# Performance work log

Measured on AMD Instinct MI355X. Metric: run time of the kernel, lower is better.

The kernel has to match this reference:

```python
import jax, jax.numpy as jnp
import numpy as np

B, L, D = 32, 2048, 768
H = 512
EPS = 1e-5  # batch_norm eps (PyG MLP default norm)


def setup_inputs() -> dict:
    key = jax.random.key(0)
    ks = jax.random.split(key, 8)
    hidden = jax.random.normal(ks[0], (B, L, D), dtype=jnp.float32)
    attention_mask = jax.random.randint(ks[1], (B, L), 0, 2, dtype=jnp.int32)
    W1 = jax.random.normal(ks[2], (D, H), dtype=jnp.float32) * 0.02
    b1 = jnp.zeros((H,), dtype=jnp.float32)
    gamma = jnp.ones((H,), dtype=jnp.float32)
    beta = jnp.zeros((H,), dtype=jnp.float32)
    W2 = jax.random.normal(ks[3], (H, H), dtype=jnp.float32) * 0.02
    b2 = jnp.zeros((H,), dtype=jnp.float32)
    return {"hidden": hidden, "attention_mask": attention_mask,
            "W1": W1, "b1": b1, "gamma": gamma, "beta": beta,
            "W2": W2, "b2": b2}


def reference(hidden, attention_mask, W1, b1, gamma, beta, W2, b2):
    # Valid-token mask; pads are excluded from the batched graph's node set.
    m = attention_mask.astype(hidden.dtype)[..., None]  # (B, L, 1)
    n_valid = jnp.maximum(jnp.sum(m), 1.0)

    # MLP layer 1: Linear -> BatchNorm (stats over all valid nodes across the
    # whole batched graph, mirroring PyG MLP training-mode batch_norm) -> ReLU
    h = jnp.einsum('bld,dh->blh', hidden, W1) + b1  # (B, L, H)
    mean = jnp.sum(h * m, axis=(0, 1)) / n_valid
    var = jnp.sum(jnp.square(h - mean) * m, axis=(0, 1)) / n_valid
    h = (h - mean) * jax.lax.rsqrt(var + EPS) * gamma + beta
    h = jax.nn.relu(h)

    # MLP layer 2 (plain_last: no norm/act)
    out = jnp.einsum('blh,hk->blk', h, W2) + b2  # (B, L, H)

    # scores == ones -> segment softmax over each sequence's valid tokens is
    # uniform 1/n_b; scatter_add over batch ids == masked mean pool.
    counts = jnp.maximum(jnp.sum(m, axis=1), 1.0)  # (B, 1)
    pooled = jnp.sum(out * m, axis=1) / counts  # (B, H)
    return pooled
```

## Files before the change

### kernel.cpp

```cpp
#include <hip/hip_runtime.h>
#include <hip/hip_bf16.h>

#define Bn 32
#define Ln 2048
#define Dn 768
#define Hn 512
#define Mn (Bn*Ln)
#define EPSC 1e-5f

#define OFF_S1   0
#define OFF_S2   512
#define OFF_SC   1024
#define OFF_SH   1536
#define OFF_CNT  2048
#define OFF_PH   2304
#define ZERO_N   (OFF_PH + Bn*Hn)
#define OFF_W1T_BYTES  131072
#define OFF_H_BYTES    1048576

#define BM 128
#define BN2 256
#define BK 64
#define LDK 72

typedef __attribute__((ext_vector_type(8))) short bf16x8;
typedef __attribute__((ext_vector_type(4))) float f32x4;

static __device__ __forceinline__ unsigned short f2bf(float x) {
  __hip_bfloat16 h = __float2bfloat16(x);
  return *reinterpret_cast<unsigned short*>(&h);
}
static __device__ __forceinline__ float bf2f(unsigned short u) {
  return __uint_as_float(((unsigned int)u) << 16);
}

__global__ void zero_kernel(float* __restrict__ p, int n) {
  int i = blockIdx.x * 256 + threadIdx.x;
  if (i < n) p[i] = 0.f;
}

__global__ void count_kernel(const int* __restrict__ mask, float* __restrict__ cnt) {
  __shared__ int red[256];
  int b = blockIdx.x, t = threadIdx.x;
  int s = 0;
#pragma unroll
  for (int i = 0; i < 8; i++) s += mask[b * Ln + i * 256 + t];
  red[t] = s;
  __syncthreads();
  for (int off = 128; off > 0; off >>= 1) {
    if (t < off) red[t] += red[t + off];
    __syncthreads();
  }
  if (t == 0) cnt[b] = (float)red[0];
}

__global__ __launch_bounds__(256) void transpose_w1(
    const float* __restrict__ W1, unsigned short* __restrict__ W1t) {
  __shared__ float tile[32][33];
  int kx = blockIdx.x * 32;
  int nx = blockIdx.y * 32;
  int tx = threadIdx.x & 31, ty = threadIdx.x >> 5;
#pragma unroll
  for (int i = 0; i < 32; i += 8)
    tile[ty + i][tx] = W1[(size_t)(kx + ty + i) * Hn + nx + tx];
  __syncthreads();
#pragma unroll
  for (int i = 0; i < 32; i += 8)
    W1t[(size_t)(nx + ty + i) * Dn + kx + tx] = f2bf(tile[tx][ty + i]);
}

__global__ __launch_bounds__(512, 4) void gemm1_mfma(
    const float* __restrict__ A, const unsigned short* __restrict__ W1t,
    const float* __restrict__ b1, const int* __restrict__ mask,
    unsigned short* __restrict__ Hout,
    float* __restrict__ gsum, float* __restrict__ gsq)
{
  __shared__ unsigned short As[BM * LDK];
  __shared__ unsigned short Bs[BN2 * LDK];
  __shared__ float csum[BN2];
  __shared__ float csq[BN2];

  const int t = threadIdx.x;
  const int bx = blockIdx.x;
  const int by = blockIdx.y;
  const int bm0 = by * BM;
  const int bn0 = bx * BN2;

  const int w = t >> 6;
  const int lane = t & 63;
  const int wm0 = (w >> 2) * 64;
  const int wn0 = (w & 3) * 64;
  const int l15 = lane & 15;
  const int quad = lane >> 4;

  const int am = t >> 2;
  const int ak = (t & 3) * 16;
  const int bn = t >> 1;
  const int bk = (t & 1) * 32;

  const float* Ap = A + (size_t)(bm0 + am) * Dn + ak;
  const unsigned short* Bp = W1t + (size_t)(bn0 + bn) * Dn + bk;

  f32x4 acc[4][4];
#pragma unroll
  for (int i = 0; i < 4; i++)
#pragma unroll
    for (int j = 0; j < 4; j++) acc[i][j] = (f32x4){0.f, 0.f, 0.f, 0.f};

  for (int k0 = 0; k0 < Dn; k0 += BK) {
    float4 a0 = *(const float4*)(Ap + k0);
    float4 a1 = *(const float4*)(Ap + k0 + 4);
    float4 a2 = *(const float4*)(Ap + k0 + 8);
    float4 a3 = *(const float4*)(Ap + k0 + 12);
    uint4 bv0 = *(const uint4*)(Bp + k0);
    uint4 bv1 = *(const uint4*)(Bp + k0 + 8);
    uint4 bv2 = *(const uint4*)(Bp + k0 + 16);
    uint4 bv3 = *(const uint4*)(Bp + k0 + 24);
    __syncthreads();
    uint4 p0, p1;
    p0.x = (unsigned int)f2bf(a0.x) | ((unsigned int)f2bf(a0.y) << 16);
    p0.y = (unsigned int)f2bf(a0.z) | ((unsigned int)f2bf(a0.w) << 16);
    p0.z = (unsigned int)f2bf(a1.x) | ((unsigned int)f2bf(a1.y) << 16);
    p0.w = (unsigned int)f2bf(a1.z) | ((unsigned int)f2bf(a1.w) << 16);
    p1.x = (unsigned int)f2bf(a2.x) | ((unsigned int)f2bf(a2.y) << 16);
    p1.y = (unsigned int)f2bf(a2.z) | ((unsigned int)f2bf(a2.w) << 16);
    p1.z = (unsigned int)f2bf(a3.x) | ((unsigned int)f2bf(a3.y) << 16);
    p1.w = (unsigned int)f2bf(a3.z) | ((unsigned int)f2bf(a3.w) << 16);
    *(uint4*)&As[am * LDK + ak] = p0;
    *(uint4*)&As[am * LDK + ak + 8] = p1;
    *(uint4*)&Bs[bn * LDK + bk] = bv0;
    *(uint4*)&Bs[bn * LDK + bk + 8] = bv1;
    *(uint4*)&Bs[bn * LDK + bk + 16] = bv2;
    *(uint4*)&Bs[bn * LDK + bk + 24] = bv3;
    __syncthreads();
#pragma unroll
    for (int s = 0; s < 2; s++) {
      bf16x8 af[4], bf[4];
#pragma unroll
      for (int mt = 0; mt < 4; mt++)
        af[mt] = *(const bf16x8*)&As[(wm0 + mt * 16 + l15) * LDK + s * 32 + quad * 8];
#pragma unroll
      for (int nt = 0; nt < 4; nt++)
        bf[nt] = *(const bf16x8*)&Bs[(wn0 + nt * 16 + l15) * LDK + s * 32 + quad * 8];
#pragma unroll
      for (int mt = 0; mt < 4; mt++)
#pragma unroll
        for (int nt = 0; nt < 4; nt++)
          acc[mt][nt] = __builtin_amdgcn_mfma_f32_16x16x32_bf16(
              af[mt], bf[nt], acc[mt][nt], 0, 0, 0);
    }
  }

  if (t < BN2) { csum[t] = 0.f; csq[t] = 0.f; }
  __syncthreads();

  float mk[4][4];
#pragma unroll
  for (int mt = 0; mt < 4; mt++) {
    int4 mv = *(const int4*)(mask + bm0 + wm0 + mt * 16 + quad * 4);
    mk[mt][0] = (float)mv.x; mk[mt][1] = (float)mv.y;
    mk[mt][2] = (float)mv.z; mk[mt][3] = (float)mv.w;
  }

  const size_t cbase = ((size_t)(by * 2 + bx)) * 32768 + (size_t)w * 4096;
#pragma unroll
  for (int nt = 0; nt < 4; nt++) {
    const int nl = wn0 + nt * 16 + l15;
    const float bias = b1[bn0 + nl];
    float ps = 0.f, pq = 0.f;
#pragma unroll
    for (int mt = 0; mt < 4; mt++) {
      ushort4 st;
      float v0 = acc[mt][nt][0] + bias;
      float v1 = acc[mt][nt][1] + bias;
      float v2 = acc[mt][nt][2] + bias;
      float v3 = acc[mt][nt][3] + bias;
      ps += v0 * mk[mt][0] + v1 * mk[mt][1] + v2 * mk[mt][2] + v3 * mk[mt][3];
      pq += v0 * v0 * mk[mt][0] + v1 * v1 * mk[mt][1] +
            v2 * v2 * mk[mt][2] + v3 * v3 * mk[mt][3];
      st.x = f2bf(v0); st.y = f2bf(v1); st.z = f2bf(v2); st.w = f2bf(v3);
      *(ushort4*)&Hout[cbase + (size_t)(mt * 4 + nt) * 256 + lane * 4] = st;
    }
    atomicAdd(&csum[nl], ps);
    atomicAdd(&csq[nl], pq);
  }

  __syncthreads();
  if (t < BN2) {
    atomicAdd(&gsum[bn0 + t], csum[t]);
    atomicAdd(&gsq[bn0 + t], csq[t]);
  }
}

__global__ void finalize_kernel(float* __restrict__ ws,
                                const float* __restrict__ gamma,
                                const float* __restrict__ beta) {
  __shared__ float nv;
  int t = threadIdx.x;
  if (t == 0) {
    float s = 0.f;
    for (int i = 0; i < Bn; i++) s += ws[OFF_CNT + i];
    nv = fmaxf(s, 1.f);
  }
  __syncthreads();
  float inv = 1.f / nv;
  float m = ws[OFF_S1 + t] * inv;
  float var = ws[OFF_S2 + t] * inv - m * m;
  float istd = rsqrtf(fmaxf(var, 0.f) + EPSC);
  float sc = istd * gamma[t];
  ws[OFF_SC + t] = sc;
  ws[OFF_SH + t] = beta[t] - m * sc;
}

__global__ __launch_bounds__(256) void bnpool_kernel(
    const unsigned short* __restrict__ Hbuf, const int* __restrict__ mask,
    const float* __restrict__ sc, const float* __restrict__ sh,
    float* __restrict__ pooled)
{
  __shared__ float pool_c[BN2];
  __shared__ float mkf[BM];
  __shared__ float scs[BN2], shs[BN2];
  const int t = threadIdx.x;
  const int chunk = blockIdx.x;
  const int by = chunk >> 1, bx = chunk & 1;
  const int b = by >> 4;
  pool_c[t] = 0.f;
  if (t < BM) mkf[t] = (float)mask[by * BM + t];
  scs[t] = sc[bx * BN2 + t];
  shs[t] = sh[bx * BN2 + t];
  __syncthreads();
  const unsigned short* base = Hbuf + (size_t)chunk * 32768;
#pragma unroll 4
  for (int i = 0; i < 32; i++) {
    int o = (i * 256 + t) * 4;
    ushort4 hv = *(const ushort4*)(base + o);
    int lane = (o >> 2) & 63;
    int mtnt = (o >> 8) & 15;
    int w = o >> 12;
    int nl = (w & 3) * 64 + (mtnt & 3) * 16 + (lane & 15);
    int ml = (w >> 2) * 64 + (mtnt >> 2) * 16 + (lane >> 4) * 4;
    float4 mv = *(const float4*)&mkf[ml];
    float scv = scs[nl], shv = shs[nl];
    float s = 0.f;
    s = fmaf(fmaxf(fmaf(bf2f(hv.x), scv, shv), 0.f), mv.x, s);
    s = fmaf(fmaxf(fmaf(bf2f(hv.y), scv, shv), 0.f), mv.y, s);
    s = fmaf(fmaxf(fmaf(bf2f(hv.z), scv, shv), 0.f), mv.z, s);
    s = fmaf(fmaxf(fmaf(bf2f(hv.w), scv, shv), 0.f), mv.w, s);
    atomicAdd(&pool_c[nl], s);
  }
  __syncthreads();
  atomicAdd(&pooled[b * Hn + bx * BN2 + t], pool_c[t]);
}

__global__ __launch_bounds__(128) void final_kernel(
    const float* __restrict__ pooledh, const float* __restrict__ cnt,
    const float* __restrict__ W2, const float* __restrict__ b2,
    float* __restrict__ out)
{
  __shared__ float pr[Hn];
  int b = blockIdx.x >> 2;
  int cc = blockIdx.x & 3;
  int t = threadIdx.x;
  float nb = cnt[b];
  float inv = 1.f / fmaxf(nb, 1.f);
#pragma unroll
  for (int i = 0; i < 4; i++)
    pr[t + i * 128] = pooledh[b * Hn + t + i * 128] * inv;
  __syncthreads();
  int c = cc * 128 + t;
  float a = 0.f;
  for (int i = 0; i < Hn; i++)
    a = fmaf(pr[i], W2[(size_t)i * Hn + c], a);
  out[b * Hn + c] = a + b2[c] * (nb * inv);
}

extern "C" void kernel_launch(void* const* d_in, const int* in_sizes, int n_in,
                              void* d_out, int out_size, void* d_ws, size_t ws_size,
                              hipStream_t stream) {
  const float* hidden = (const float*)d_in[0];
  const int*   mask   = (const int*)d_in[1];
  const float* W1     = (const float*)d_in[2];
  const float* b1     = (const float*)d_in[3];
  const float* gamma  = (const float*)d_in[4];
  const float* beta   = (const float*)d_in[5];
  const float* W2     = (const float*)d_in[6];
  const float* b2     = (const float*)d_in[7];
  float* out = (float*)d_out;
  float* ws  = (float*)d_ws;
  unsigned short* W1t  = (unsigned short*)((char*)d_ws + OFF_W1T_BYTES);
  unsigned short* Hbuf = (unsigned short*)((char*)d_ws + OFF_H_BYTES);

  zero_kernel<<<(ZERO_N + 255) / 256, 256, 0, stream>>>(ws, ZERO_N);
  count_kernel<<<Bn, 256, 0, stream>>>(mask, ws + OFF_CNT);
  transpose_w1<<<dim3(Dn / 32, Hn / 32), 256, 0, stream>>>(W1, W1t);
  gemm1_mfma<<<dim3(Hn / BN2, Mn / BM), 512, 0, stream>>>(
      hidden, W1t, b1, mask, Hbuf, ws + OFF_S1, ws + OFF_S2);
  finalize_kernel<<<1, Hn, 0, stream>>>(ws, gamma, beta);
  bnpool_kernel<<<(Mn / BM) * (Hn / BN2), 256, 0, stream>>>(
      Hbuf, mask, ws + OFF_SC, ws + OFF_SH, ws + OFF_PH);
  final_kernel<<<Bn * 4, 128, 0, stream>>>(ws + OFF_PH, ws + OFF_CNT, W2, b2, out);
}
```

Measured before the change: 421.7 us.

## Shrink GEMM tile to 128x128, fuse launch prologue and BN finalize into pool

The first GEMM tile drops from 128x256 with 512 threads to 128x128 with 256 threads, and the occupancy hint changes. The zero and count kernels merge into one pre-kernel, and the BN finalize moves into the pool kernel so two launches disappear. The pool kernel now reduces per thread in registers and then across warps in shared memory, replacing per-element shared atomics. The final matvec uses four independent accumulators. Smaller tiles re-read the A matrix twice as often, and every pool block recomputes the scale and shift.

```diff
diff --git a/kernel.cpp b/kernel.cpp
--- a/kernel.cpp
+++ b/kernel.cpp
@@ -10,16 +10,13 @@
 
 #define OFF_S1   0
 #define OFF_S2   512
-#define OFF_SC   1024
-#define OFF_SH   1536
 #define OFF_CNT  2048
 #define OFF_PH   2304
-#define ZERO_N   (OFF_PH + Bn*Hn)
 #define OFF_W1T_BYTES  131072
 #define OFF_H_BYTES    1048576
 
 #define BM 128
-#define BN2 256
+#define BN2 128
 #define BK 64
 #define LDK 72
 
@@ -30,28 +27,34 @@
   __hip_bfloat16 h = __float2bfloat16(x);
   return *reinterpret_cast<unsigned short*>(&h);
 }
+static __device__ __forceinline__ unsigned int pk2(float lo, float hi) {
+  return (unsigned int)f2bf(lo) | ((unsigned int)f2bf(hi) << 16);
+}
 static __device__ __forceinline__ float bf2f(unsigned short u) {
   return __uint_as_float(((unsigned int)u) << 16);
 }
 
-__global__ void zero_kernel(float* __restrict__ p, int n) {
-  int i = blockIdx.x * 256 + threadIdx.x;
-  if (i < n) p[i] = 0.f;
-}
-
-__global__ void count_kernel(const int* __restrict__ mask, float* __restrict__ cnt) {
-  __shared__ int red[256];
-  int b = blockIdx.x, t = threadIdx.x;
-  int s = 0;
-#pragma unroll
-  for (int i = 0; i < 8; i++) s += mask[b * Ln + i * 256 + t];
-  red[t] = s;
-  __syncthreads();
-  for (int off = 128; off > 0; off >>= 1) {
-    if (t < off) red[t] += red[t + off];
+__global__ __launch_bounds__(256) void pre_kernel(const int* __restrict__ mask,
+                                                  float* __restrict__ ws) {
+  int blk = blockIdx.x, t = threadIdx.x;
+  if (blk < Bn) {
+    __shared__ int red[256];
+    int s = 0;
+#pragma unroll
+    for (int i = 0; i < 8; i++) s += mask[blk * Ln + i * 256 + t];
+    red[t] = s;
     __syncthreads();
-  }
-  if (t == 0) cnt[b] = (float)red[0];
+    for (int off = 128; off > 0; off >>= 1) {
+      if (t < off) red[t] += red[t + off];
+      __syncthreads();
+    }
+    if (t == 0) ws[OFF_CNT + blk] = (float)red[0];
+  } else {
+#pragma unroll
+    for (int i = 0; i < 4; i++) ws[OFF_S1 + i * 256 + t] = 0.f;
+#pragma unroll
+    for (int i = 0; i < 64; i++) ws[OFF_PH + i * 256 + t] = 0.f;
+  }
 }
 
 __global__ __launch_bounds__(256) void transpose_w1(
@@ -69,7 +72,7 @@
     W1t[(size_t)(nx + ty + i) * Dn + kx + tx] = f2bf(tile[tx][ty + i]);
 }
 
-__global__ __launch_bounds__(512, 4) void gemm1_mfma(
+__global__ __launch_bounds__(256, 3) void gemm1_mfma(
     const float* __restrict__ A, const unsigned short* __restrict__ W1t,
     const float* __restrict__ b1, const int* __restrict__ mask,
     unsigned short* __restrict__ Hout,
@@ -88,18 +91,16 @@
 
   const int w = t >> 6;
   const int lane = t & 63;
-  const int wm0 = (w >> 2) * 64;
-  const int wn0 = (w & 3) * 64;
+  const int wm0 = (w >> 1) * 64;
+  const int wn0 = (w & 1) * 64;
   const int l15 = lane & 15;
   const int quad = lane >> 4;
 
-  const int am = t >> 2;
-  const int ak = (t & 3) * 16;
-  const int bn = t >> 1;
-  const int bk = (t & 1) * 32;
+  const int am = t >> 1;
+  const int ak = (t & 1) * 32;
 
   const float* Ap = A + (size_t)(bm0 + am) * Dn + ak;
-  const unsigned short* Bp = W1t + (size_t)(bn0 + bn) * Dn + bk;
+  const unsigned short* Bp = W1t + (size_t)(bn0 + am) * Dn + ak;
 
   f32x4 acc[4][4];
 #pragma unroll
@@ -108,30 +109,23 @@
     for (int j = 0; j < 4; j++) acc[i][j] = (f32x4){0.f, 0.f, 0.f, 0.f};
 
   for (int k0 = 0; k0 < Dn; k0 += BK) {
-    float4 a0 = *(const float4*)(Ap + k0);
-    float4 a1 = *(const float4*)(Ap + k0 + 4);
-    float4 a2 = *(const float4*)(Ap + k0 + 8);
-    float4 a3 = *(const float4*)(Ap + k0 + 12);
-    uint4 bv0 = *(const uint4*)(Bp + k0);
-    uint4 bv1 = *(const uint4*)(Bp + k0 + 8);
-    uint4 bv2 = *(const uint4*)(Bp + k0 + 16);
-    uint4 bv3 = *(const uint4*)(Bp + k0 + 24);
+    float4 av[8];
+#pragma unroll
+    for (int i = 0; i < 8; i++) av[i] = *(const float4*)(Ap + k0 + i * 4);
+    uint4 bv[4];
+#pragma unroll
+    for (int j = 0; j < 4; j++) bv[j] = *(const uint4*)(Bp + k0 + j * 8);
     __syncthreads();
-    uint4 p0, p1;
-    p0.x = (unsigned int)f2bf(a0.x) | ((unsigned int)f2bf(a0.y) << 16);
-    p0.y = (unsigned int)f2bf(a0.z) | ((unsigned int)f2bf(a0.w) << 16);
-    p0.z = (unsigned int)f2bf(a1.x) | ((unsigned int)f2bf(a1.y) << 16);
-    p0.w = (unsigned int)f2bf(a1.z) | ((unsigned int)f2bf(a1.w) << 16);
-    p1.x = (unsigned int)f2bf(a2.x) | ((unsigned int)f2bf(a2.y) << 16);
-    p1.y = (unsigned int)f2bf(a2.z) | ((unsigned int)f2bf(a2.w) << 16);
-    p1.z = (unsigned int)f2bf(a3.x) | ((unsigned int)f2bf(a3.y) << 16);
-    p1.w = (unsigned int)f2bf(a3.z) | ((unsigned int)f2bf(a3.w) << 16);
-    *(uint4*)&As[am * LDK + ak] = p0;
-    *(uint4*)&As[am * LDK + ak + 8] = p1;
-    *(uint4*)&Bs[bn * LDK + bk] = bv0;
-    *(uint4*)&Bs[bn * LDK + bk + 8] = bv1;
-    *(uint4*)&Bs[bn * LDK + bk + 16] = bv2;
-    *(uint4*)&Bs[bn * LDK + bk + 24] = bv3;
+#pragma unroll
+    for (int j = 0; j < 4; j++) {
+      uint4 pa;
+      pa.x = pk2(av[2 * j].x, av[2 * j].y);
+      pa.y = pk2(av[2 * j].z, av[2 * j].w);
+      pa.z = pk2(av[2 * j + 1].x, av[2 * j + 1].y);
+      pa.w = pk2(av[2 * j + 1].z, av[2 * j + 1].w);
+      *(uint4*)&As[am * LDK + ak + j * 8] = pa;
+      *(uint4*)&Bs[am * LDK + ak + j * 8] = bv[j];
+    }
     __syncthreads();
 #pragma unroll
     for (int s = 0; s < 2; s++) {
@@ -162,7 +156,7 @@
     mk[mt][2] = (float)mv.z; mk[mt][3] = (float)mv.w;
   }
 
-  const size_t cbase = ((size_t)(by * 2 + bx)) * 32768 + (size_t)w * 4096;
+  const size_t cbase = ((size_t)(by * 4 + bx)) * 16384 + (size_t)w * 4096;
 #pragma unroll
   for (int nt = 0; nt < 4; nt++) {
     const int nl = wn0 + nt * 16 + l15;
@@ -192,64 +186,63 @@
   }
 }
 
-__global__ void finalize_kernel(float* __restrict__ ws,
-                                const float* __restrict__ gamma,
-                                const float* __restrict__ beta) {
-  __shared__ float nv;
-  int t = threadIdx.x;
-  if (t == 0) {
-    float s = 0.f;
-    for (int i = 0; i < Bn; i++) s += ws[OFF_CNT + i];
-    nv = fmaxf(s, 1.f);
-  }
-  __syncthreads();
-  float inv = 1.f / nv;
-  float m = ws[OFF_S1 + t] * inv;
-  float var = ws[OFF_S2 + t] * inv - m * m;
-  float istd = rsqrtf(fmaxf(var, 0.f) + EPSC);
-  float sc = istd * gamma[t];
-  ws[OFF_SC + t] = sc;
-  ws[OFF_SH + t] = beta[t] - m * sc;
-}
-
 __global__ __launch_bounds__(256) void bnpool_kernel(
     const unsigned short* __restrict__ Hbuf, const int* __restrict__ mask,
-    const float* __restrict__ sc, const float* __restrict__ sh,
-    float* __restrict__ pooled)
+    const float* __restrict__ ws, const float* __restrict__ gamma,
+    const float* __restrict__ beta, float* __restrict__ PH)
 {
-  __shared__ float pool_c[BN2];
   __shared__ float mkf[BM];
   __shared__ float scs[BN2], shs[BN2];
+  __shared__ float part[4][64];
+  __shared__ float redc[32];
   const int t = threadIdx.x;
   const int chunk = blockIdx.x;
-  const int by = chunk >> 1, bx = chunk & 1;
+  const int by = chunk >> 2, bx = chunk & 3;
   const int b = by >> 4;
-  pool_c[t] = 0.f;
+  if (t < 32) redc[t] = ws[OFF_CNT + t];
   if (t < BM) mkf[t] = (float)mask[by * BM + t];
-  scs[t] = sc[bx * BN2 + t];
-  shs[t] = sh[bx * BN2 + t];
-  __syncthreads();
-  const unsigned short* base = Hbuf + (size_t)chunk * 32768;
-#pragma unroll 4
-  for (int i = 0; i < 32; i++) {
-    int o = (i * 256 + t) * 4;
-    ushort4 hv = *(const ushort4*)(base + o);
-    int lane = (o >> 2) & 63;
-    int mtnt = (o >> 8) & 15;
-    int w = o >> 12;
-    int nl = (w & 3) * 64 + (mtnt & 3) * 16 + (lane & 15);
-    int ml = (w >> 2) * 64 + (mtnt >> 2) * 16 + (lane >> 4) * 4;
-    float4 mv = *(const float4*)&mkf[ml];
-    float scv = scs[nl], shv = shs[nl];
-    float s = 0.f;
-    s = fmaf(fmaxf(fmaf(bf2f(hv.x), scv, shv), 0.f), mv.x, s);
-    s = fmaf(fmaxf(fmaf(bf2f(hv.y), scv, shv), 0.f), mv.y, s);
-    s = fmaf(fmaxf(fmaf(bf2f(hv.z), scv, shv), 0.f), mv.z, s);
-    s = fmaf(fmaxf(fmaf(bf2f(hv.w), scv, shv), 0.f), mv.w, s);
-    atomicAdd(&pool_c[nl], s);
-  }
-  __syncthreads();
-  atomicAdd(&pooled[b * Hn + bx * BN2 + t], pool_c[t]);
+  __syncthreads();
+  if (t < BN2) {
+    float nv = 0.f;
+#pragma unroll
+    for (int i = 0; i < 32; i++) nv += redc[i];
+    nv = fmaxf(nv, 1.f);
+    float inv = 1.f / nv;
+    int c = bx * BN2 + t;
+    float m = ws[OFF_S1 + c] * inv;
+    float var = ws[OFF_S2 + c] * inv - m * m;
+    float istd = rsqrtf(fmaxf(var, 0.f) + EPSC);
+    float sc = istd * gamma[c];
+    scs[t] = sc;
+    shs[t] = beta[c] - m * sc;
+  }
+  __syncthreads();
+
+  const int l15 = t & 15, nt = (t >> 4) & 3, w = t >> 6;
+  const int wn0 = (w & 1) * 64, wm0 = (w >> 1) * 64;
+  const int nl = wn0 + nt * 16 + l15;
+  const float scv = scs[nl], shv = shs[nl];
+  const unsigned short* base =
+      Hbuf + (size_t)chunk * 16384 + (size_t)w * 4096 + nt * 256 + l15 * 4;
+  float acc = 0.f;
+#pragma unroll
+  for (int mt = 0; mt < 4; mt++)
+#pragma unroll
+    for (int q = 0; q < 4; q++) {
+      ushort4 hv = *(const ushort4*)(base + mt * 1024 + q * 64);
+      const float* mv = &mkf[wm0 + mt * 16 + q * 4];
+      acc += fmaxf(fmaf(bf2f(hv.x), scv, shv), 0.f) * mv[0]
+           + fmaxf(fmaf(bf2f(hv.y), scv, shv), 0.f) * mv[1]
+           + fmaxf(fmaf(bf2f(hv.z), scv, shv), 0.f) * mv[2]
+           + fmaxf(fmaf(bf2f(hv.w), scv, shv), 0.f) * mv[3];
+    }
+  part[w][nt * 16 + l15] = acc;
+  __syncthreads();
+  if (t < BN2) {
+    int half = t >> 6, cl = t & 63;
+    float v = part[half][cl] + part[half + 2][cl];
+    atomicAdd(&PH[b * Hn + bx * BN2 + t], v);
+  }
 }
 
 __global__ __launch_bounds__(128) void final_kernel(
@@ -268,10 +261,14 @@
     pr[t + i * 128] = pooledh[b * Hn + t + i * 128] * inv;
   __syncthreads();
   int c = cc * 128 + t;
-  float a = 0.f;
-  for (int i = 0; i < Hn; i++)
-    a = fmaf(pr[i], W2[(size_t)i * Hn + c], a);
-  out[b * Hn + c] = a + b2[c] * (nb * inv);
+  float a0 = 0.f, a1 = 0.f, a2 = 0.f, a3 = 0.f;
+  for (int i = 0; i < Hn; i += 4) {
+    a0 = fmaf(pr[i],     W2[(size_t)i * Hn + c],       a0);
+    a1 = fmaf(pr[i + 1], W2[(size_t)(i + 1) * Hn + c], a1);
+    a2 = fmaf(pr[i + 2], W2[(size_t)(i + 2) * Hn + c], a2);
+    a3 = fmaf(pr[i + 3], W2[(size_t)(i + 3) * Hn + c], a3);
+  }
+  out[b * Hn + c] = (a0 + a1) + (a2 + a3) + b2[c] * (nb * inv);
 }
 
 extern "C" void kernel_launch(void* const* d_in, const int* in_sizes, int n_in,
@@ -290,13 +287,11 @@
   unsigned short* W1t  = (unsigned short*)((char*)d_ws + OFF_W1T_BYTES);
   unsigned short* Hbuf = (unsigned short*)((char*)d_ws + OFF_H_BYTES);
 
-  zero_kernel<<<(ZERO_N + 255) / 256, 256, 0, stream>>>(ws, ZERO_N);
-  count_kernel<<<Bn, 256, 0, stream>>>(mask, ws + OFF_CNT);
+  pre_kernel<<<Bn + 1, 256, 0, stream>>>(mask, ws);
   transpose_w1<<<dim3(Dn / 32, Hn / 32), 256, 0, stream>>>(W1, W1t);
-  gemm1_mfma<<<dim3(Hn / BN2, Mn / BM), 512, 0, stream>>>(
+  gemm1_mfma<<<dim3(Hn / BN2, Mn / BM), 256, 0, stream>>>(
       hidden, W1t, b1, mask, Hbuf, ws + OFF_S1, ws + OFF_S2);
-  finalize_kernel<<<1, Hn, 0, stream>>>(ws, gamma, beta);
   bnpool_kernel<<<(Mn / BM) * (Hn / BN2), 256, 0, stream>>>(
-      Hbuf, mask, ws + OFF_SC, ws + OFF_SH, ws + OFF_PH);
+      Hbuf, mask, ws, gamma, beta, ws + OFF_PH);
   final_kernel<<<Bn * 4, 128, 0, stream>>>(ws + OFF_PH, ws + OFF_CNT, W2, b2, out);
 }
```

Result: slower. 566.8 us (+34.4%).
